# Optimization experiments

Hardware: AMD Instinct MI355X
Metric: run time of the kernel (lower is better)

Reference implementation:

```python
import jax, jax.numpy as jnp
import numpy as np

CROSS_NUM, EXPERT_NUM, LOW_RANK = 3, 4, 64
BATCH, DIM = 32768, 512


def setup_inputs() -> dict:
    key = jax.random.key(0)
    ks = jax.random.split(key, 6)
    s = 0.05  # small init so tanh stays in its linear-ish range
    return {
        "x": jax.random.normal(ks[0], (BATCH, DIM), dtype=jnp.float32),
        "Vs": jax.random.normal(ks[1], (CROSS_NUM, EXPERT_NUM, LOW_RANK, DIM), dtype=jnp.float32) * s,
        "Cs": jax.random.normal(ks[2], (CROSS_NUM, EXPERT_NUM, LOW_RANK, LOW_RANK), dtype=jnp.float32) * s,
        "Us": jax.random.normal(ks[3], (CROSS_NUM, EXPERT_NUM, DIM, LOW_RANK), dtype=jnp.float32) * s,
        "bias": jax.random.normal(ks[4], (CROSS_NUM, DIM), dtype=jnp.float32) * s,
        "gate_w": jax.random.normal(ks[5], (DIM, EXPERT_NUM), dtype=jnp.float32) * s,
    }


def reference(x, Vs, Cs, Us, bias, gate_w):
    # x: [B, D]. The original keeps a trailing singleton axis; we drop it and
    # batch the per-expert einsum chain over the expert axis e.
    x0 = x
    x_l = x
    for i in range(CROSS_NUM):
        # gating (shared Dense(1) per expert, applied to current x_l): [B, E]
        g = x_l @ gate_w
        # low-rank expert chain, batched over experts
        v = jnp.tanh(jnp.einsum('eld,bd->bel', Vs[i], x_l))   # [B, E, low]
        c = jnp.tanh(jnp.einsum('elk,bek->bel', Cs[i], v))    # [B, E, low]
        u = jnp.einsum('edl,bel->bed', Us[i], c)              # [B, E, D]
        expert_out = (u + bias[i][None, None, :]) * x0[:, None, :]  # [B, E, D]
        # mixture combine (raw gating scores, no softmax, as in original)
        moe = jnp.einsum('bed,be->bd', expert_out, g)
        x_l = moe + x_l
    return x_l
```

## Files before the change

kernel.cpp:

```cpp
#include <hip/hip_runtime.h>
#include <hip/hip_bf16.h>


#define CROSS   3
#define ENUM    4
#define LR      64
#define ELD     256
#define DIM     512
#define BATCH   32768
#define BT      64
#define NTHR    1024

#define XL_W    520
#define Y_W     264

typedef __bf16 bf16x8 __attribute__((ext_vector_type(8)));
typedef float  f32x4  __attribute__((ext_vector_type(4)));
typedef unsigned short us;
typedef unsigned short us4 __attribute__((ext_vector_type(4)));

__device__ __forceinline__ us f2bf(float f) {
    return __builtin_bit_cast(us, (__bf16)f);
}
__device__ __forceinline__ float bf2f(us b) {
    unsigned int u = ((unsigned int)b) << 16;
    return __builtin_bit_cast(float, u);
}
__device__ __forceinline__ float tanh_fast(float x) {
    float t = __expf(2.f * x);
    return (t - 1.f) * __builtin_amdgcn_rcpf(t + 1.f);
}

#define MFMA(a, b, c) __builtin_amdgcn_mfma_f32_16x16x32_bf16(a, b, c, 0, 0, 0)

__device__ __forceinline__ void gload_lds16(const us* g, us* l) {
    __builtin_amdgcn_global_load_lds(
        (const __attribute__((address_space(1))) unsigned int*)g,
        (__attribute__((address_space(3))) unsigned int*)l, 16, 0, 0);
}

__global__ __launch_bounds__(64) void swz_all(
    const float* __restrict__ Vs, const float* __restrict__ Cs,
    const float* __restrict__ Us, const float* __restrict__ gw,
    us* __restrict__ Vf, us* __restrict__ Cf,
    us* __restrict__ Uf, us* __restrict__ Gf)
{
    int b = blockIdx.x;
    int lane = threadIdx.x;
    if (b < 768) {
        int i = b >> 8, t = b & 255;
        int nt = t >> 4, ks = t & 15;
        int n  = nt * 16 + (lane & 15);
        int k0 = ks * 32 + (lane >> 4) * 8;
        const float* src = Vs + (size_t)i * ELD * DIM + (size_t)n * DIM + k0;
        us* dst = Vf + (size_t)i * ELD * DIM
                + ((size_t)(nt * 16 + ks) * 64 + lane) * 8;
        #pragma unroll
        for (int j = 0; j < 8; ++j) dst[j] = f2bf(src[j]);
    } else if (b < 1536) {
        int bb = b - 768;
        int i = bb >> 8, t = bb & 255;
        int nt = t >> 3, ks = t & 7;
        int n  = nt * 16 + (lane & 15);
        int k0 = ks * 32 + (lane >> 4) * 8;
        int e = k0 >> 6, l0 = k0 & 63;
        const float* src = Us + (size_t)i * ENUM * DIM * LR
                         + (size_t)e * DIM * LR + (size_t)n * LR + l0;
        us* dst = Uf + (size_t)i * DIM * ELD
                + ((size_t)(nt * 8 + ks) * 64 + lane) * 8;
        #pragma unroll
        for (int j = 0; j < 8; ++j) dst[j] = f2bf(src[j]);
    } else if (b < 1632) {
        int bb = b - 1536;
        int i = bb >> 5, rest = bb & 31;
        int e = rest >> 3, t = rest & 7;
        int nt = t >> 1, ks = t & 1;
        int n  = nt * 16 + (lane & 15);
        int k0 = ks * 32 + (lane >> 4) * 8;
        const float* src = Cs + (((size_t)(i * ENUM + e) * LR + n) * LR) + k0;
        us* dst = Cf + (size_t)i * ENUM * LR * LR
                + ((size_t)((e * 4 + nt) * 2 + ks) * 64 + lane) * 8;
        #pragma unroll
        for (int j = 0; j < 8; ++j) dst[j] = f2bf(src[j]);
    } else {
        int ks = b - 1632;
        int n  = lane & 15;
        int k0 = ks * 32 + (lane >> 4) * 8;
        us* dst = Gf + ((size_t)ks * 64 + lane) * 8;
        #pragma unroll
        for (int j = 0; j < 8; ++j)
            dst[j] = (n < ENUM) ? f2bf(gw[(size_t)(k0 + j) * ENUM + n]) : (us)0;
    }
}

__global__ __launch_bounds__(NTHR, 4) void dcn_fused(
    const float* __restrict__ x,
    float* __restrict__ out,
    const us* __restrict__ Vf,
    const us* __restrict__ Cf,
    const us* __restrict__ Uf,
    const us* __restrict__ Gf,
    const float* __restrict__ bias)
{
    __shared__ us xl_s[BT * XL_W];
    __shared__ us y_s[BT * Y_W];
    __shared__ us wst[16384];
    __shared__ float g_s[BT * ENUM];

    const int tid  = threadIdx.x;
    const int wave = tid >> 6, lane = tid & 63;
    const int quad = lane >> 4, nl = lane & 15;
    const int rh = wave >> 3, wc = wave & 7;
    const int rh32 = rh * 32;
    const int row0 = blockIdx.x * BT;

    #pragma unroll
    for (int it = 0; it < 8; ++it) {
        int f4 = tid + it * NTHR;
        int r = f4 >> 7, c4 = f4 & 127;
        float4 v = *reinterpret_cast<const float4*>(
            x + (size_t)(row0 + r) * DIM + c4 * 4);
        us4 p;
        p[0] = f2bf(v.x); p[1] = f2bf(v.y); p[2] = f2bf(v.z); p[3] = f2bf(v.w);
        *reinterpret_cast<us4*>(&xl_s[r * XL_W + c4 * 4]) = p;
    }
    __syncthreads();

    unsigned int x0p[2][4][2];
    #pragma unroll
    for (int mt = 0; mt < 2; ++mt)
        #pragma unroll
        for (int nt = 0; nt < 4; ++nt) {
            int rb = rh32 + mt * 16 + quad * 4;
            int col = wc * 64 + nt * 16 + nl;
            unsigned int b0 = xl_s[(rb + 0) * XL_W + col];
            unsigned int b1 = xl_s[(rb + 1) * XL_W + col];
            unsigned int b2 = xl_s[(rb + 2) * XL_W + col];
            unsigned int b3 = xl_s[(rb + 3) * XL_W + col];
            x0p[mt][nt][0] = b0 | (b1 << 16);
            x0p[mt][nt][1] = b2 | (b3 << 16);
        }

    const int e = wc >> 1, h = wc & 1;

    #pragma unroll 1
    for (int layer = 0; layer < CROSS; ++layer) {
        const us* Vl = Vf + (size_t)layer * ELD * DIM;
        const us* Cl = Cf + (size_t)layer * ENUM * LR * LR;
        const us* Ul = Uf + (size_t)layer * DIM * ELD;
        const float* bl = bias + layer * DIM;

        bf16x8 creg[2][2];
        #pragma unroll
        for (int ks = 0; ks < 2; ++ks)
            #pragma unroll
            for (int nt = 0; nt < 2; ++nt)
                creg[ks][nt] = *reinterpret_cast<const bf16x8*>(
                    &Cl[((size_t)((e * 4 + h * 2 + nt) * 2 + ks) * 64 + lane) * 8]);

        gload_lds16(Vl + ((size_t)(wave * 16 + 0) * 64 + lane) * 8,
                    wst + wave * 512);
        __syncthreads();

        f32x4 acc1[2][2];
        f32x4 gacc[2];
        #pragma unroll
        for (int mt = 0; mt < 2; ++mt) {
            gacc[mt] = (f32x4)0.f;
            acc1[mt][0] = (f32x4)0.f;
            acc1[mt][1] = (f32x4)0.f;
        }
        #pragma unroll 2
        for (int ks = 0; ks < 16; ++ks) {
            if (ks < 15)
                gload_lds16(Vl + ((size_t)(wave * 16 + ks + 1) * 64 + lane) * 8,
                            wst + ((ks + 1) & 1) * 8192 + wave * 512);
            const us* vb = wst + (ks & 1) * 8192;
            bf16x8 a0 = *reinterpret_cast<const bf16x8*>(
                &xl_s[(rh32 + nl) * XL_W + ks * 32 + quad * 8]);
            bf16x8 a1 = *reinterpret_cast<const bf16x8*>(
                &xl_s[(rh32 + 16 + nl) * XL_W + ks * 32 + quad * 8]);
            #pragma unroll
            for (int nt = 0; nt < 2; ++nt) {
                bf16x8 bfr = *reinterpret_cast<const bf16x8*>(
                    &vb[(wc * 2 + nt) * 512 + lane * 8]);
                acc1[0][nt] = MFMA(a0, bfr, acc1[0][nt]);
                acc1[1][nt] = MFMA(a1, bfr, acc1[1][nt]);
            }
            if (wc == 0) {
                bf16x8 bg = *reinterpret_cast<const bf16x8*>(
                    &Gf[((size_t)ks * 64 + lane) * 8]);
                gacc[0] = MFMA(a0, bg, gacc[0]);
                gacc[1] = MFMA(a1, bg, gacc[1]);
            }
            if (ks < 15) __syncthreads();
        }
        #pragma unroll
        for (int mt = 0; mt < 2; ++mt)
            #pragma unroll
            for (int r = 0; r < 4; ++r) {
                int row = rh32 + mt * 16 + quad * 4 + r;
                #pragma unroll
                for (int nt = 0; nt < 2; ++nt)
                    y_s[row * Y_W + wc * 32 + nt * 16 + nl] =
                        f2bf(tanh_fast(acc1[mt][nt][r]));
            }
        if (wc == 0 && nl < ENUM) {
            #pragma unroll
            for (int mt = 0; mt < 2; ++mt)
                #pragma unroll
                for (int r = 0; r < 4; ++r)
                    g_s[(rh32 + mt * 16 + quad * 4 + r) * ENUM + nl] =
                        gacc[mt][r];
        }
        __syncthreads();

        float Gv[2][4];
        #pragma unroll
        for (int mt = 0; mt < 2; ++mt)
            #pragma unroll
            for (int r = 0; r < 4; ++r) {
                int row = rh32 + mt * 16 + quad * 4 + r;
                f32x4 g4 = *reinterpret_cast<const f32x4*>(&g_s[row * ENUM]);
                Gv[mt][r] = g4[0] + g4[1] + g4[2] + g4[3];
            }

        f32x4 acc2[2][2];
        #pragma unroll
        for (int mt = 0; mt < 2; ++mt) {
            acc2[mt][0] = (f32x4)0.f;
            acc2[mt][1] = (f32x4)0.f;
        }
        #pragma unroll
        for (int ks = 0; ks < 2; ++ks) {
            bf16x8 a0 = *reinterpret_cast<const bf16x8*>(
                &y_s[(rh32 + nl) * Y_W + e * 64 + ks * 32 + quad * 8]);
            bf16x8 a1 = *reinterpret_cast<const bf16x8*>(
                &y_s[(rh32 + 16 + nl) * Y_W + e * 64 + ks * 32 + quad * 8]);
            #pragma unroll
            for (int nt = 0; nt < 2; ++nt) {
                acc2[0][nt] = MFMA(a0, creg[ks][nt], acc2[0][nt]);
                acc2[1][nt] = MFMA(a1, creg[ks][nt], acc2[1][nt]);
            }
        }
        gload_lds16(Ul + ((size_t)(wave * 8 + 0) * 64 + lane) * 8,
                    wst + wave * 512);
        gload_lds16(Ul + ((size_t)((wave + 16) * 8 + 0) * 64 + lane) * 8,
                    wst + (wave + 16) * 512);
        __syncthreads();
        #pragma unroll
        for (int mt = 0; mt < 2; ++mt)
            #pragma unroll
            for (int r = 0; r < 4; ++r) {
                int row = rh32 + mt * 16 + quad * 4 + r;
                float gv = g_s[row * ENUM + e];
                #pragma unroll
                for (int nt = 0; nt < 2; ++nt)
                    y_s[row * Y_W + e * 64 + h * 32 + nt * 16 + nl] =
                        f2bf(tanh_fast(acc2[mt][nt][r]) * gv);
            }
        __syncthreads();

        f32x4 acc3[2][4];
        #pragma unroll
        for (int mt = 0; mt < 2; ++mt)
            #pragma unroll
            for (int nt = 0; nt < 4; ++nt) acc3[mt][nt] = (f32x4)0.f;
        #pragma unroll 1
        for (int ks = 0; ks < 8; ++ks) {
            if (ks > 0) {
                __syncthreads();
                gload_lds16(Ul + ((size_t)(wave * 8 + ks) * 64 + lane) * 8,
                            wst + wave * 512);
                gload_lds16(Ul + ((size_t)((wave + 16) * 8 + ks) * 64 + lane) * 8,
                            wst + (wave + 16) * 512);
                __syncthreads();
            }
            bf16x8 a0 = *reinterpret_cast<const bf16x8*>(
                &y_s[(rh32 + nl) * Y_W + ks * 32 + quad * 8]);
            bf16x8 a1 = *reinterpret_cast<const bf16x8*>(
                &y_s[(rh32 + 16 + nl) * Y_W + ks * 32 + quad * 8]);
            #pragma unroll
            for (int nt = 0; nt < 4; ++nt) {
                bf16x8 bfr = *reinterpret_cast<const bf16x8*>(
                    &wst[(wc * 4 + nt) * 512 + lane * 8]);
                acc3[0][nt] = MFMA(a0, bfr, acc3[0][nt]);
                acc3[1][nt] = MFMA(a1, bfr, acc3[1][nt]);
            }
        }
        __syncthreads();

        #pragma unroll
        for (int nt = 0; nt < 4; ++nt) {
            int col = wc * 64 + nt * 16 + nl;
            float bc = bl[col];
            #pragma unroll
            for (int mt = 0; mt < 2; ++mt)
                #pragma unroll
                for (int r = 0; r < 4; ++r) {
                    int row = rh32 + mt * 16 + quad * 4 + r;
                    float x0v = bf2f(
                        (us)(x0p[mt][nt][r >> 1] >> ((r & 1) * 16)));
                    float xlo = bf2f(xl_s[row * XL_W + col]);
                    float res = xlo
                              + x0v * (acc3[mt][nt][r] + bc * Gv[mt][r]);
                    if (layer == CROSS - 1)
                        out[(size_t)(row0 + row) * DIM + col] = res;
                    else
                        xl_s[row * XL_W + col] = f2bf(res);
                }
        }
    }
}

extern "C" void kernel_launch(void* const* d_in, const int* in_sizes, int n_in,
                              void* d_out, int out_size, void* d_ws,
                              size_t ws_size, hipStream_t stream) {
    const float* x      = (const float*)d_in[0];
    const float* Vs     = (const float*)d_in[1];
    const float* Cs     = (const float*)d_in[2];
    const float* Us     = (const float*)d_in[3];
    const float* bias   = (const float*)d_in[4];
    const float* gate_w = (const float*)d_in[5];
    float* out = (float*)d_out;

    us* Vf = (us*)d_ws;
    us* Uf = Vf + (size_t)CROSS * ELD * DIM;
    us* Cf = Uf + (size_t)CROSS * DIM * ELD;
    us* Gf = Cf + (size_t)CROSS * ENUM * LR * LR;

    swz_all<<<1648, 64, 0, stream>>>(Vs, Cs, Us, gate_w, Vf, Cf, Uf, Gf);
    dcn_fused<<<BATCH / BT, NTHR, 0, stream>>>(x, out, Vf, Cf, Uf, Gf, bias);
}
```

Baseline: 318.1 us.

## Halve block tile and use per-wave triple-buffered weight streaming without block barriers

Shrinks the block to 32 rows and 8 waves, and gives each wave a private 3-slot LDS ring. V and U fragments are streamed into it with global_load_lds and drained with explicit vmcnt waits, replacing the block-wide __syncthreads per k-step. The gate scores are now computed by a scalar dot product from an LDS copy of gate_w instead of an extra MFMA on one wave, and bias is hoisted into registers. Each block now reloads the full weights for only half as many rows, which doubles weight traffic per row, in exchange for removing barrier stalls and allowing more blocks per CU.

```diff
diff --git a/kernel.cpp b/kernel.cpp
--- a/kernel.cpp
+++ b/kernel.cpp
@@ -8,8 +8,8 @@
 #define ELD     256
 #define DIM     512
 #define BATCH   32768
-#define BT      64
-#define NTHR    1024
+#define BT      32
+#define NTHR    512
 
 #define XL_W    520
 #define Y_W     264
@@ -39,11 +39,16 @@
         (__attribute__((address_space(3))) unsigned int*)l, 16, 0, 0);
 }
 
+__device__ __forceinline__ void wait_slot(int left) {
+    if (left >= 2)      asm volatile("s_waitcnt vmcnt(2)" ::: "memory");
+    else if (left == 1) asm volatile("s_waitcnt vmcnt(1)" ::: "memory");
+    else                asm volatile("s_waitcnt vmcnt(0)" ::: "memory");
+}
+
 __global__ __launch_bounds__(64) void swz_all(
     const float* __restrict__ Vs, const float* __restrict__ Cs,
-    const float* __restrict__ Us, const float* __restrict__ gw,
-    us* __restrict__ Vf, us* __restrict__ Cf,
-    us* __restrict__ Uf, us* __restrict__ Gf)
+    const float* __restrict__ Us,
+    us* __restrict__ Vf, us* __restrict__ Cf, us* __restrict__ Uf)
 {
     int b = blockIdx.x;
     int lane = threadIdx.x;
@@ -70,7 +75,7 @@
                 + ((size_t)(nt * 8 + ks) * 64 + lane) * 8;
         #pragma unroll
         for (int j = 0; j < 8; ++j) dst[j] = f2bf(src[j]);
-    } else if (b < 1632) {
+    } else {
         int bb = b - 1536;
         int i = bb >> 5, rest = bb & 31;
         int e = rest >> 3, t = rest & 7;
@@ -82,14 +87,6 @@
                 + ((size_t)((e * 4 + nt) * 2 + ks) * 64 + lane) * 8;
         #pragma unroll
         for (int j = 0; j < 8; ++j) dst[j] = f2bf(src[j]);
-    } else {
-        int ks = b - 1632;
-        int n  = lane & 15;
-        int k0 = ks * 32 + (lane >> 4) * 8;
-        us* dst = Gf + ((size_t)ks * 64 + lane) * 8;
-        #pragma unroll
-        for (int j = 0; j < 8; ++j)
-            dst[j] = (n < ENUM) ? f2bf(gw[(size_t)(k0 + j) * ENUM + n]) : (us)0;
     }
 }
 
@@ -99,20 +96,28 @@
     const us* __restrict__ Vf,
     const us* __restrict__ Cf,
     const us* __restrict__ Uf,
-    const us* __restrict__ Gf,
+    const float* __restrict__ gw,
     const float* __restrict__ bias)
 {
     __shared__ us xl_s[BT * XL_W];
     __shared__ us y_s[BT * Y_W];
-    __shared__ us wst[16384];
-    __shared__ float g_s[BT * ENUM];
+    __shared__ us wst[8 * 1536];
+    __shared__ us gw_s[4 * 512];
+    __shared__ __align__(16) float g_s[BT * ENUM];
+    __shared__ __align__(16) float sc[NTHR];
 
     const int tid  = threadIdx.x;
     const int wave = tid >> 6, lane = tid & 63;
     const int quad = lane >> 4, nl = lane & 15;
-    const int rh = wave >> 3, wc = wave & 7;
-    const int rh32 = rh * 32;
+    const int wc   = wave;
     const int row0 = blockIdx.x * BT;
+
+#define ISSUE_V(f) gload_lds16( \
+    Vl + ((size_t)((wc * 2 + ((f) & 1)) * 16 + ((f) >> 1)) * 64 + lane) * 8, \
+    &wst[wave * 1536 + ((f) % 3) * 512])
+#define ISSUE_U(f) gload_lds16( \
+    Ul + ((size_t)((wc * 4 + ((f) & 3)) * 8 + ((f) >> 2)) * 64 + lane) * 8, \
+    &wst[wave * 1536 + ((f) % 3) * 512])
 
     #pragma unroll
     for (int it = 0; it < 8; ++it) {
@@ -124,6 +129,12 @@
         p[0] = f2bf(v.x); p[1] = f2bf(v.y); p[2] = f2bf(v.z); p[3] = f2bf(v.w);
         *reinterpret_cast<us4*>(&xl_s[r * XL_W + c4 * 4]) = p;
     }
+    #pragma unroll
+    for (int j = 0; j < 4; ++j) {
+        int idx = tid * 4 + j;
+        int e = idx >> 9, d = idx & 511;
+        gw_s[idx] = f2bf(gw[(size_t)d * ENUM + e]);
+    }
     __syncthreads();
 
     unsigned int x0p[2][4][2];
@@ -131,7 +142,7 @@
     for (int mt = 0; mt < 2; ++mt)
         #pragma unroll
         for (int nt = 0; nt < 4; ++nt) {
-            int rb = rh32 + mt * 16 + quad * 4;
+            int rb = mt * 16 + quad * 4;
             int col = wc * 64 + nt * 16 + nl;
             unsigned int b0 = xl_s[(rb + 0) * XL_W + col];
             unsigned int b1 = xl_s[(rb + 1) * XL_W + col];
@@ -157,62 +168,67 @@
             for (int nt = 0; nt < 2; ++nt)
                 creg[ks][nt] = *reinterpret_cast<const bf16x8*>(
                     &Cl[((size_t)((e * 4 + h * 2 + nt) * 2 + ks) * 64 + lane) * 8]);
-
-        gload_lds16(Vl + ((size_t)(wave * 16 + 0) * 64 + lane) * 8,
-                    wst + wave * 512);
-        __syncthreads();
+        float bias_r[4];
+        #pragma unroll
+        for (int nt = 0; nt < 4; ++nt)
+            bias_r[nt] = bl[wc * 64 + nt * 16 + nl];
+
+        ISSUE_V(0); ISSUE_V(1); ISSUE_V(2);
+        __syncthreads();
+
+        {
+            int grow = tid >> 4, ge = (tid >> 2) & 3, gq = tid & 3;
+            float gp = 0.f;
+            #pragma unroll
+            for (int dd = 0; dd < 16; ++dd) {
+                int d0 = gq * 128 + ((dd + gq * 4) & 15) * 8;
+                bf16x8 xa = *reinterpret_cast<const bf16x8*>(
+                    &xl_s[grow * XL_W + d0]);
+                bf16x8 wa = *reinterpret_cast<const bf16x8*>(
+                    &gw_s[ge * 512 + d0]);
+                #pragma unroll
+                for (int j = 0; j < 8; ++j)
+                    gp += (float)xa[j] * (float)wa[j];
+            }
+            sc[tid] = gp;
+        }
+        __syncthreads();
+        if (tid < 128)
+            g_s[tid] = sc[tid * 4] + sc[tid * 4 + 1]
+                     + sc[tid * 4 + 2] + sc[tid * 4 + 3];
 
         f32x4 acc1[2][2];
-        f32x4 gacc[2];
-        #pragma unroll
-        for (int mt = 0; mt < 2; ++mt) {
-            gacc[mt] = (f32x4)0.f;
-            acc1[mt][0] = (f32x4)0.f;
-            acc1[mt][1] = (f32x4)0.f;
-        }
-        #pragma unroll 2
+        acc1[0][0] = (f32x4)0.f; acc1[0][1] = (f32x4)0.f;
+        acc1[1][0] = (f32x4)0.f; acc1[1][1] = (f32x4)0.f;
+        #pragma unroll
         for (int ks = 0; ks < 16; ++ks) {
-            if (ks < 15)
-                gload_lds16(Vl + ((size_t)(wave * 16 + ks + 1) * 64 + lane) * 8,
-                            wst + ((ks + 1) & 1) * 8192 + wave * 512);
-            const us* vb = wst + (ks & 1) * 8192;
             bf16x8 a0 = *reinterpret_cast<const bf16x8*>(
-                &xl_s[(rh32 + nl) * XL_W + ks * 32 + quad * 8]);
+                &xl_s[(nl) * XL_W + ks * 32 + quad * 8]);
             bf16x8 a1 = *reinterpret_cast<const bf16x8*>(
-                &xl_s[(rh32 + 16 + nl) * XL_W + ks * 32 + quad * 8]);
+                &xl_s[(16 + nl) * XL_W + ks * 32 + quad * 8]);
             #pragma unroll
             for (int nt = 0; nt < 2; ++nt) {
-                bf16x8 bfr = *reinterpret_cast<const bf16x8*>(
-                    &vb[(wc * 2 + nt) * 512 + lane * 8]);
-                acc1[0][nt] = MFMA(a0, bfr, acc1[0][nt]);
-                acc1[1][nt] = MFMA(a1, bfr, acc1[1][nt]);
-            }
-            if (wc == 0) {
-                bf16x8 bg = *reinterpret_cast<const bf16x8*>(
-                    &Gf[((size_t)ks * 64 + lane) * 8]);
-                gacc[0] = MFMA(a0, bg, gacc[0]);
-                gacc[1] = MFMA(a1, bg, gacc[1]);
-            }
-            if (ks < 15) __syncthreads();
+                const int f = ks * 2 + nt;
+                wait_slot(31 - f);
+                __builtin_amdgcn_sched_barrier(0);
+                bf16x8 b = *reinterpret_cast<const bf16x8*>(
+                    &wst[wave * 1536 + (f % 3) * 512 + lane * 8]);
+                acc1[0][nt] = MFMA(a0, b, acc1[0][nt]);
+                acc1[1][nt] = MFMA(a1, b, acc1[1][nt]);
+                __builtin_amdgcn_sched_barrier(0);
+                if (f + 3 < 32) { ISSUE_V(f + 3); }
+            }
         }
         #pragma unroll
         for (int mt = 0; mt < 2; ++mt)
             #pragma unroll
             for (int r = 0; r < 4; ++r) {
-                int row = rh32 + mt * 16 + quad * 4 + r;
+                int row = mt * 16 + quad * 4 + r;
                 #pragma unroll
                 for (int nt = 0; nt < 2; ++nt)
                     y_s[row * Y_W + wc * 32 + nt * 16 + nl] =
                         f2bf(tanh_fast(acc1[mt][nt][r]));
             }
-        if (wc == 0 && nl < ENUM) {
-            #pragma unroll
-            for (int mt = 0; mt < 2; ++mt)
-                #pragma unroll
-                for (int r = 0; r < 4; ++r)
-                    g_s[(rh32 + mt * 16 + quad * 4 + r) * ENUM + nl] =
-                        gacc[mt][r];
-        }
         __syncthreads();
 
         float Gv[2][4];
@@ -220,39 +236,34 @@
         for (int mt = 0; mt < 2; ++mt)
             #pragma unroll
             for (int r = 0; r < 4; ++r) {
-                int row = rh32 + mt * 16 + quad * 4 + r;
+                int row = mt * 16 + quad * 4 + r;
                 f32x4 g4 = *reinterpret_cast<const f32x4*>(&g_s[row * ENUM]);
                 Gv[mt][r] = g4[0] + g4[1] + g4[2] + g4[3];
             }
 
+        ISSUE_U(0); ISSUE_U(1); ISSUE_U(2);
+
         f32x4 acc2[2][2];
-        #pragma unroll
-        for (int mt = 0; mt < 2; ++mt) {
-            acc2[mt][0] = (f32x4)0.f;
-            acc2[mt][1] = (f32x4)0.f;
-        }
+        acc2[0][0] = (f32x4)0.f; acc2[0][1] = (f32x4)0.f;
+        acc2[1][0] = (f32x4)0.f; acc2[1][1] = (f32x4)0.f;
         #pragma unroll
         for (int ks = 0; ks < 2; ++ks) {
             bf16x8 a0 = *reinterpret_cast<const bf16x8*>(
-                &y_s[(rh32 + nl) * Y_W + e * 64 + ks * 32 + quad * 8]);
+                &y_s[(nl) * Y_W + e * 64 + ks * 32 + quad * 8]);
             bf16x8 a1 = *reinterpret_cast<const bf16x8*>(
-                &y_s[(rh32 + 16 + nl) * Y_W + e * 64 + ks * 32 + quad * 8]);
+                &y_s[(16 + nl) * Y_W + e * 64 + ks * 32 + quad * 8]);
             #pragma unroll
             for (int nt = 0; nt < 2; ++nt) {
                 acc2[0][nt] = MFMA(a0, creg[ks][nt], acc2[0][nt]);
                 acc2[1][nt] = MFMA(a1, creg[ks][nt], acc2[1][nt]);
             }
         }
-        gload_lds16(Ul + ((size_t)(wave * 8 + 0) * 64 + lane) * 8,
-                    wst + wave * 512);
-        gload_lds16(Ul + ((size_t)((wave + 16) * 8 + 0) * 64 + lane) * 8,
-                    wst + (wave + 16) * 512);
         __syncthreads();
         #pragma unroll
         for (int mt = 0; mt < 2; ++mt)
             #pragma unroll
             for (int r = 0; r < 4; ++r) {
-                int row = rh32 + mt * 16 + quad * 4 + r;
+                int row = mt * 16 + quad * 4 + r;
                 float gv = g_s[row * ENUM + e];
                 #pragma unroll
                 for (int nt = 0; nt < 2; ++nt)
@@ -266,44 +277,39 @@
         for (int mt = 0; mt < 2; ++mt)
             #pragma unroll
             for (int nt = 0; nt < 4; ++nt) acc3[mt][nt] = (f32x4)0.f;
-        #pragma unroll 1
+        #pragma unroll
         for (int ks = 0; ks < 8; ++ks) {
-            if (ks > 0) {
-                __syncthreads();
-                gload_lds16(Ul + ((size_t)(wave * 8 + ks) * 64 + lane) * 8,
-                            wst + wave * 512);
-                gload_lds16(Ul + ((size_t)((wave + 16) * 8 + ks) * 64 + lane) * 8,
-                            wst + (wave + 16) * 512);
-                __syncthreads();
-            }
             bf16x8 a0 = *reinterpret_cast<const bf16x8*>(
-                &y_s[(rh32 + nl) * Y_W + ks * 32 + quad * 8]);
+                &y_s[(nl) * Y_W + ks * 32 + quad * 8]);
             bf16x8 a1 = *reinterpret_cast<const bf16x8*>(
-                &y_s[(rh32 + 16 + nl) * Y_W + ks * 32 + quad * 8]);
+                &y_s[(16 + nl) * Y_W + ks * 32 + quad * 8]);
             #pragma unroll
             for (int nt = 0; nt < 4; ++nt) {
-                bf16x8 bfr = *reinterpret_cast<const bf16x8*>(
-                    &wst[(wc * 4 + nt) * 512 + lane * 8]);
-                acc3[0][nt] = MFMA(a0, bfr, acc3[0][nt]);
-                acc3[1][nt] = MFMA(a1, bfr, acc3[1][nt]);
-            }
-        }
-        __syncthreads();
+                const int f = ks * 4 + nt;
+                wait_slot(31 - f);
+                __builtin_amdgcn_sched_barrier(0);
+                bf16x8 b = *reinterpret_cast<const bf16x8*>(
+                    &wst[wave * 1536 + (f % 3) * 512 + lane * 8]);
+                acc3[0][nt] = MFMA(a0, b, acc3[0][nt]);
+                acc3[1][nt] = MFMA(a1, b, acc3[1][nt]);
+                __builtin_amdgcn_sched_barrier(0);
+                if (f + 3 < 32) { ISSUE_U(f + 3); }
+            }
+        }
 
         #pragma unroll
         for (int nt = 0; nt < 4; ++nt) {
             int col = wc * 64 + nt * 16 + nl;
-            float bc = bl[col];
             #pragma unroll
             for (int mt = 0; mt < 2; ++mt)
                 #pragma unroll
                 for (int r = 0; r < 4; ++r) {
-                    int row = rh32 + mt * 16 + quad * 4 + r;
+                    int row = mt * 16 + quad * 4 + r;
                     float x0v = bf2f(
                         (us)(x0p[mt][nt][r >> 1] >> ((r & 1) * 16)));
                     float xlo = bf2f(xl_s[row * XL_W + col]);
                     float res = xlo
-                              + x0v * (acc3[mt][nt][r] + bc * Gv[mt][r]);
+                              + x0v * (acc3[mt][nt][r] + bias_r[nt] * Gv[mt][r]);
                     if (layer == CROSS - 1)
                         out[(size_t)(row0 + row) * DIM + col] = res;
                     else
@@ -311,6 +317,8 @@
                 }
         }
     }
+#undef ISSUE_V
+#undef ISSUE_U
 }
 
 extern "C" void kernel_launch(void* const* d_in, const int* in_sizes, int n_in,
@@ -327,8 +335,8 @@
     us* Vf = (us*)d_ws;
     us* Uf = Vf + (size_t)CROSS * ELD * DIM;
     us* Cf = Uf + (size_t)CROSS * DIM * ELD;
-    us* Gf = Cf + (size_t)CROSS * ENUM * LR * LR;
-
-    swz_all<<<1648, 64, 0, stream>>>(Vs, Cs, Us, gate_w, Vf, Cf, Uf, Gf);
-    dcn_fused<<<BATCH / BT, NTHR, 0, stream>>>(x, out, Vf, Cf, Uf, Gf, bias);
-}
+
+    swz_all<<<1632, 64, 0, stream>>>(Vs, Cs, Us, Vf, Cf, Uf);
+    dcn_fused<<<BATCH / BT, NTHR, 0, stream>>>(x, out, Vf, Cf, Uf,
+                                               gate_w, bias);
+}
```

Result: slower. 359.8 us (+13.1%).
